# Kernel optimization log

Measured on AMD Instinct MI355X. Metric: run time of the kernel, lower is better.

The kernel has to match this reference:

```python
import jax, jax.numpy as jnp
import numpy as np

DIM = 2048
NUM_HEADS = 16
HEAD_DIM = DIM // NUM_HEADS
ROPE_BASE = 10000.0


def _rope_tables(seq_len, head_dim, dtype):
    # inv_freq over even indices, emb = cat(freqs, freqs) as in RoPEPositionalEncoding
    inv_freq = 1.0 / (ROPE_BASE ** (jnp.arange(0, head_dim, 2, dtype=jnp.float32) / head_dim))
    t = jnp.arange(seq_len, dtype=jnp.float32)
    freqs = jnp.outer(t, inv_freq)                      # [S, D/2]
    emb = jnp.concatenate([freqs, freqs], axis=-1)      # [S, D]
    # add head axis so tables broadcast over [B, S, H, D]
    return jnp.cos(emb)[:, None, :].astype(dtype), jnp.sin(emb)[:, None, :].astype(dtype)


def _apply_rope(x, cos, sin):
    # x: [B, S, H, D]; cos/sin: [S, 1, D]
    x1, x2 = x[..., ::2], x[..., 1::2]
    rotated = jnp.concatenate([-x2, x1], axis=-1)
    return x * cos + rotated * sin


def setup_inputs() -> dict:
    key = jax.random.key(0)
    ks = jax.random.split(key, 5)
    B, S = 2, 2048
    s = 1.0 / np.sqrt(DIM)
    return {
        "x": jax.random.normal(ks[0], (B, S, DIM), dtype=jnp.float32),
        "Wq": jax.random.normal(ks[1], (DIM, DIM), dtype=jnp.float32) * s,
        "Wk": jax.random.normal(ks[2], (DIM, DIM), dtype=jnp.float32) * s,
        "Wv": jax.random.normal(ks[3], (DIM, DIM), dtype=jnp.float32) * s,
        "Wo": jax.random.normal(ks[4], (DIM, DIM), dtype=jnp.float32) * s,
    }


def reference(x, Wq, Wk, Wv, Wo):
    B, S, _ = x.shape
    H, D = NUM_HEADS, HEAD_DIM
    scale = D ** -0.5

    q = (x @ Wq.T).reshape(B, S, H, D)
    k = (x @ Wk.T).reshape(B, S, H, D)
    v = (x @ Wv.T).reshape(B, S, H, D)

    cos, sin = _rope_tables(S, D, x.dtype)
    q = _apply_rope(q, cos, sin)
    k = _apply_rope(k, cos, sin)

    # [B, H, S, D]
    q = q.transpose(0, 2, 1, 3)
    k = k.transpose(0, 2, 1, 3)
    v = v.transpose(0, 2, 1, 3)

    scores = jnp.einsum("bhqd,bhkd->bhqk", q, k) * scale
    causal = jnp.tril(jnp.ones((S, S), dtype=bool))
    scores = jnp.where(causal, scores, -jnp.inf)
    attn = jax.nn.softmax(scores, axis=-1)

    out = jnp.einsum("bhqk,bhkd->bhqd", attn, v)
    out = out.transpose(0, 2, 1, 3).reshape(B, S, H * D)
    return out @ Wo.T
```

## Files before the change

kernel.cpp:

```cpp
#include <hip/hip_runtime.h>
#include <math.h>

#define DIM   2048
#define NH    16
#define HD    128
#define BB    2
#define SS    2048
#define MTOT  4096
#define NT    32

typedef unsigned short u16;
typedef short bf16x8 __attribute__((ext_vector_type(8)));
typedef float f32x4  __attribute__((ext_vector_type(4)));

typedef const void __attribute__((address_space(1)))* gas_ptr;
typedef void __attribute__((address_space(3)))* las_ptr;

__device__ __forceinline__ u16 f2bf(float f){
  union { float f; unsigned u; } v; v.f = f;
  unsigned r = v.u + 0x7FFFu + ((v.u >> 16) & 1u);
  return (u16)(r >> 16);
}
__device__ __forceinline__ float bf2f(u16 h){
  union { unsigned u; float f; } v; v.u = ((unsigned)h) << 16;
  return v.f;
}

__global__ __launch_bounds__(256) void cvt_all(
    const float* __restrict__ x,  const float* __restrict__ wq,
    const float* __restrict__ wk, const float* __restrict__ wv,
    u16* __restrict__ xb, u16* __restrict__ w0, u16* __restrict__ w1, u16* __restrict__ w2){
  int i = blockIdx.x * 256 + threadIdx.x;
  const float* src; u16* dst; int j;
  if (i < 2097152) { src = x; dst = xb; j = i; }
  else {
    int k = i - 2097152;
    int seg = k >> 20;
    j = k & 1048575;
    src = (seg == 0) ? wq : (seg == 1 ? wk : wv);
    dst = (seg == 0) ? w0 : (seg == 1 ? w1 : w2);
  }
  float4 v = ((const float4*)src)[j];
  ushort4 o;
  o.x = f2bf(v.x); o.y = f2bf(v.y); o.z = f2bf(v.z); o.w = f2bf(v.w);
  ((ushort4*)dst)[j] = o;
}

__global__ __launch_bounds__(256) void cvt_kernel(const float* __restrict__ in,
                                                  u16* __restrict__ out, int n4){
  int i = blockIdx.x * blockDim.x + threadIdx.x;
  if (i >= n4) return;
  float4 v = ((const float4*)in)[i];
  ushort4 o;
  o.x = f2bf(v.x); o.y = f2bf(v.y); o.z = f2bf(v.z); o.w = f2bf(v.w);
  ((ushort4*)out)[i] = o;
}

template<bool STORE_BF16>
__global__ __launch_bounds__(512, 2) void gemm256(
    const u16* __restrict__ A,
    const u16* __restrict__ B0, const u16* __restrict__ B1, const u16* __restrict__ B2,
    void* __restrict__ C0, void* __restrict__ C1, void* __restrict__ C2)
{
  __shared__ __align__(16) u16 Ar[2][2][256 * 32];
  __shared__ __align__(16) u16 Br[2][2][256 * 32];

  const int tid  = threadIdx.x;
  const int lane = tid & 63;
  const int wave = tid >> 6;
  const int wm   = wave >> 2;
  const int wn   = wave & 3;
  const int lg   = lane >> 4;
  const int lr   = lane & 15;

  const int cpx = gridDim.x >> 3;
  const int wg  = (blockIdx.x & 7) * cpx + (blockIdx.x >> 3);
  const int z   = wg >> 7;
  const int rem = wg & 127;
  const int m0  = (rem >> 3) * 256;
  const int n0  = (rem & 7) * 256;

  const u16* Bm = (z == 0) ? B0 : (z == 1 ? B1 : B2);
  void* Cm      = (z == 0) ? C0 : (z == 1 ? C1 : C2);
  const u16* Asrc = A  + (size_t)m0 * DIM;
  const u16* Bsrc = Bm + (size_t)n0 * DIM;

  f32x4 acc[8][4];
#pragma unroll
  for (int m = 0; m < 8; ++m)
#pragma unroll
    for (int n = 0; n < 4; ++n) acc[m][n] = (f32x4)0.0f;
  bf16x8 breg[4];

  auto stage = [&](const u16* src, u16* ldsreg, int kabs) {
#pragma unroll
    for (int it = 0; it < 2; ++it) {
      int c   = it * 512 + tid;
      int st  = c >> 4;
      int row = ((st >> 2) << 4) + (c & 15);
      int k   = kabs + ((st & 3) << 3);
      const u16* g = src + (size_t)row * DIM + k;
      char* l = (char*)ldsreg + (it * 512 + wave * 64) * 16;
      __builtin_amdgcn_global_load_lds((gas_ptr)g, (las_ptr)l, 16, 0, 0);
    }
  };

  stage(Asrc, Ar[0][0], 0);
  stage(Bsrc, Br[0][0], 0);
  stage(Asrc, Ar[0][1], 32);
  stage(Bsrc, Br[0][1], 32);
  asm volatile("s_waitcnt vmcnt(4)" ::: "memory");
  __builtin_amdgcn_s_barrier();

#define GPHASE(QQ, KK, GG)                                                              \
  {                                                                                     \
    const u16* Ab_ = Ar[b][KK];                                                         \
    const u16* Bb_ = Br[b][KK];                                                         \
    bf16x8 a0 = *(const bf16x8*)((const char*)Ab_ + ((((wm*8 + GG*4 + 0)*4 + lg) << 8) + (lr << 4))); \
    bf16x8 a1 = *(const bf16x8*)((const char*)Ab_ + ((((wm*8 + GG*4 + 1)*4 + lg) << 8) + (lr << 4))); \
    bf16x8 a2 = *(const bf16x8*)((const char*)Ab_ + ((((wm*8 + GG*4 + 2)*4 + lg) << 8) + (lr << 4))); \
    bf16x8 a3 = *(const bf16x8*)((const char*)Ab_ + ((((wm*8 + GG*4 + 3)*4 + lg) << 8) + (lr << 4))); \
    if (GG == 0) {                                                                      \
      _Pragma("unroll")                                                                 \
      for (int n_ = 0; n_ < 4; ++n_)                                                    \
        breg[n_] = *(const bf16x8*)((const char*)Bb_ + ((((wn*4 + n_)*4 + lg) << 8) + (lr << 4))); \
    }                                                                                   \
    if (t + 1 < NT) {                                                                   \
      if (QQ == 0) stage(Asrc, Ar[b ^ 1][0], (t + 1) * 64);                             \
      if (QQ == 1) stage(Bsrc, Br[b ^ 1][0], (t + 1) * 64);                             \
      if (QQ == 2) stage(Asrc, Ar[b ^ 1][1], (t + 1) * 64 + 32);                        \
      if (QQ == 3) stage(Bsrc, Br[b ^ 1][1], (t + 1) * 64 + 32);                        \
    }                                                                                   \
    __builtin_amdgcn_s_barrier();                                                       \
    asm volatile("s_waitcnt lgkmcnt(0)" ::: "memory");                                  \
    __builtin_amdgcn_sched_barrier(0);                                                  \
    __builtin_amdgcn_s_setprio(1);                                                      \
    {                                                                                   \
      acc[GG*4+0][0] = __builtin_amdgcn_mfma_f32_16x16x32_bf16(a0, breg[0], acc[GG*4+0][0], 0,0,0); \
      acc[GG*4+0][1] = __builtin_amdgcn_mfma_f32_16x16x32_bf16(a0, breg[1], acc[GG*4+0][1], 0,0,0); \
      acc[GG*4+0][2] = __builtin_amdgcn_mfma_f32_16x16x32_bf16(a0, breg[2], acc[GG*4+0][2], 0,0,0); \
      acc[GG*4+0][3] = __builtin_amdgcn_mfma_f32_16x16x32_bf16(a0, breg[3], acc[GG*4+0][3], 0,0,0); \
      acc[GG*4+1][0] = __builtin_amdgcn_mfma_f32_16x16x32_bf16(a1, breg[0], acc[GG*4+1][0], 0,0,0); \
      acc[GG*4+1][1] = __builtin_amdgcn_mfma_f32_16x16x32_bf16(a1, breg[1], acc[GG*4+1][1], 0,0,0); \
      acc[GG*4+1][2] = __builtin_amdgcn_mfma_f32_16x16x32_bf16(a1, breg[2], acc[GG*4+1][2], 0,0,0); \
      acc[GG*4+1][3] = __builtin_amdgcn_mfma_f32_16x16x32_bf16(a1, breg[3], acc[GG*4+1][3], 0,0,0); \
      acc[GG*4+2][0] = __builtin_amdgcn_mfma_f32_16x16x32_bf16(a2, breg[0], acc[GG*4+2][0], 0,0,0); \
      acc[GG*4+2][1] = __builtin_amdgcn_mfma_f32_16x16x32_bf16(a2, breg[1], acc[GG*4+2][1], 0,0,0); \
      acc[GG*4+2][2] = __builtin_amdgcn_mfma_f32_16x16x32_bf16(a2, breg[2], acc[GG*4+2][2], 0,0,0); \
      acc[GG*4+2][3] = __builtin_amdgcn_mfma_f32_16x16x32_bf16(a2, breg[3], acc[GG*4+2][3], 0,0,0); \
      acc[GG*4+3][0] = __builtin_amdgcn_mfma_f32_16x16x32_bf16(a3, breg[0], acc[GG*4+3][0], 0,0,0); \
      acc[GG*4+3][1] = __builtin_amdgcn_mfma_f32_16x16x32_bf16(a3, breg[1], acc[GG*4+3][1], 0,0,0); \
      acc[GG*4+3][2] = __builtin_amdgcn_mfma_f32_16x16x32_bf16(a3, breg[2], acc[GG*4+3][2], 0,0,0); \
      acc[GG*4+3][3] = __builtin_amdgcn_mfma_f32_16x16x32_bf16(a3, breg[3], acc[GG*4+3][3], 0,0,0); \
    }                                                                                   \
    __builtin_amdgcn_s_setprio(0);                                                      \
    if (QQ == 1) {                                                                      \
      if (t + 1 < NT) { asm volatile("s_waitcnt vmcnt(4)" ::: "memory"); }              \
      else            { asm volatile("s_waitcnt vmcnt(0)" ::: "memory"); }              \
    }                                                                                   \
    if (QQ == 3) {                                                                      \
      if (t + 1 < NT) { asm volatile("s_waitcnt vmcnt(4)" ::: "memory"); }              \
    }                                                                                   \
    __builtin_amdgcn_s_barrier();                                                       \
  }

  for (int t = 0; t < NT; ++t) {
    const int b = t & 1;
    GPHASE(0, 0, 0)
    GPHASE(1, 0, 1)
    GPHASE(2, 1, 0)
    GPHASE(3, 1, 1)
  }
#undef GPHASE

#pragma unroll
  for (int mf = 0; mf < 8; ++mf) {
    int grow = m0 + wm * 128 + mf * 16 + lg * 4;
#pragma unroll
    for (int nf = 0; nf < 4; ++nf) {
      int gcol = n0 + wn * 64 + nf * 16 + lr;
#pragma unroll
      for (int r = 0; r < 4; ++r) {
        float val = acc[mf][nf][r];
        if (STORE_BF16) ((u16*)Cm)[(size_t)(grow + r) * DIM + gcol]   = f2bf(val);
        else            ((float*)Cm)[(size_t)(grow + r) * DIM + gcol] = val;
      }
    }
  }
}

__global__ __launch_bounds__(256) void rope_kernel(u16* __restrict__ Q, u16* __restrict__ Kt){
  int gid  = blockIdx.x * 4 + (threadIdx.x >> 6);
  int lane = threadIdx.x & 63;
  int h = gid & (NH - 1);
  int s = (gid >> 4) & (SS - 1);
  int b = gid >> 15;
  size_t base = ((size_t)(b * SS + s)) * DIM + (size_t)h * HD;

  float ang = (float)s * __expf(-(float)lane * 0.14391156831212787f);
  float c, sn;
  sincosf(ang, &sn, &c);
  int jh = lane >> 1;
  int par = lane & 1;

  unsigned pq = *(const unsigned*)(Q + base + 2 * lane);
  float qe = bf2f((u16)(pq & 0xffff)), qo = bf2f((u16)(pq >> 16));
  float qa  = __shfl(qe, jh),      qb  = __shfl(qo, jh);
  float qa2 = __shfl(qe, 32 + jh), qb2 = __shfl(qo, 32 + jh);
  float qxj   = par ? qb  : qa;
  float qxj64 = par ? qb2 : qa2;
  u16 q_lo = f2bf(qxj   * c - qo * sn);
  u16 q_hi = f2bf(qxj64 * c + qe * sn);

  unsigned pk = *(const unsigned*)(Kt + base + 2 * lane);
  float ke = bf2f((u16)(pk & 0xffff)), ko = bf2f((u16)(pk >> 16));
  float ka  = __shfl(ke, jh),      kb  = __shfl(ko, jh);
  float ka2 = __shfl(ke, 32 + jh), kb2 = __shfl(ko, 32 + jh);
  float kxj   = par ? kb  : ka;
  float kxj64 = par ? kb2 : ka2;
  u16 k_lo = f2bf(kxj   * c - ko * sn);
  u16 k_hi = f2bf(kxj64 * c + ke * sn);

  Q [base + lane] = q_lo;  Q [base + 64 + lane] = q_hi;
  Kt[base + lane] = k_lo;  Kt[base + 64 + lane] = k_hi;
}

__global__ __launch_bounds__(256) void transpose_v(const u16* __restrict__ V,
                                                   u16* __restrict__ VT){
  __shared__ __align__(16) u16 T[64 * 64];
  const int tid = threadIdx.x;
  const int s0 = blockIdx.x * 64;
  const int d0 = blockIdx.y * 64;
  const int bh = blockIdx.z;
  const int b = bh >> 4, h = bh & 15;

#pragma unroll
  for (int it = 0; it < 2; ++it) {
    int c = it * 256 + tid;
    int s = c >> 3, cc = c & 7;
    uint4 v = *(const uint4*)(V + (size_t)(b * SS + s0 + s) * DIM + h * HD + d0 + cc * 8);
    *(uint4*)((char*)T + s * 128 + (((cc ^ (s & 7)) & 7) << 4)) = v;
  }
  __syncthreads();
#pragma unroll
  for (int it = 0; it < 2; ++it) {
    int c = it * 256 + tid;
    int d = c >> 3, sc = c & 7;
    u16 tmp[8];
#pragma unroll
    for (int j = 0; j < 8; ++j) {
      int s = sc * 8 + j;
      tmp[j] = *(const u16*)((char*)T + s * 128 + ((((d >> 3) ^ (s & 7)) & 7) << 4) + (d & 7) * 2);
    }
    *(uint4*)(VT + (size_t)bh * HD * SS + (size_t)(d0 + d) * SS + s0 + sc * 8) = *(const uint4*)tmp;
  }
}

#define SCALE 0.08838834764831845f

__global__ __launch_bounds__(512) void attn_kernel(
    const u16* __restrict__ Q, const u16* __restrict__ Kg, const u16* __restrict__ VT,
    u16* __restrict__ AO)
{
  __shared__ __align__(16) u16 Klds[2][64 * 128];
  __shared__ __align__(16) u16 Vlds[2][128 * 64];
  __shared__ __align__(16) u16 Plds[8][16 * 64];

  const int tid  = threadIdx.x;
  const int lane = tid & 63;
  const int w    = tid >> 6;
  const int lg   = lane >> 4;
  const int lr   = lane & 15;
  const int pair = blockIdx.x;
  const int bh   = blockIdx.y;
  const int b    = bh >> 4, h = bh & 15;
  const size_t headoff = (size_t)b * SS * DIM + (size_t)h * HD;
  const u16* VTh = VT + (size_t)bh * HD * SS;

  for (int half = 0; half < 2; ++half) {
    const int Qt = half ? (15 - pair) : pair;
    const int qbase = Qt * 128;
    const int nkv = Qt * 2 + 2;

    bf16x8 qf[4];
    {
      const u16* qrow = Q + headoff + (size_t)(qbase + w * 16 + lr) * DIM;
#pragma unroll
      for (int kf = 0; kf < 4; ++kf)
        qf[kf] = *(const bf16x8*)(qrow + kf * 32 + lg * 8);
    }

    f32x4 o_acc[8];
#pragma unroll
    for (int nf = 0; nf < 8; ++nf) o_acc[nf] = (f32x4)0.0f;
    float mrow[4] = {-INFINITY, -INFINITY, -INFINITY, -INFINITY};
    float lrow[4] = {0.f, 0.f, 0.f, 0.f};

    int cur = 0;

#define STAGE(BUF, T)                                                              \
    {                                                                              \
      const int kv0s = (T) * 64;                                                   \
      _Pragma("unroll")                                                            \
      for (int it = 0; it < 2; ++it) {                                             \
        int c = it * 512 + tid;                                                    \
        int r = c >> 4, slot = c & 15;                                             \
        int cc = slot ^ (r & 7);                                                   \
        const u16* ga = Kg + headoff + (size_t)(kv0s + r) * DIM + cc * 8;          \
        char* la = (char*)Klds[BUF] + (it * 512 + w * 64) * 16;                    \
        __builtin_amdgcn_global_load_lds((gas_ptr)ga, (las_ptr)la, 16, 0, 0);      \
      }                                                                            \
      _Pragma("unroll")                                                            \
      for (int it = 0; it < 2; ++it) {                                             \
        int c = it * 512 + tid;                                                    \
        int d = c >> 3, slot = c & 7;                                              \
        int cc = slot ^ (d & 7);                                                   \
        const u16* gv = VTh + (size_t)d * SS + kv0s + cc * 8;                      \
        char* lv = (char*)Vlds[BUF] + (it * 512 + w * 64) * 16;                    \
        __builtin_amdgcn_global_load_lds((gas_ptr)gv, (las_ptr)lv, 16, 0, 0);      \
      }                                                                            \
    }

    STAGE(0, 0);
    __syncthreads();

    for (int t = 0; t < nkv; ++t) {
      const int kv0 = t * 64;
      if (t + 1 < nkv) STAGE(cur ^ 1, t + 1);

      if (kv0 <= qbase + w * 16 + 15) {
        f32x4 sacc[4];
#pragma unroll
        for (int sf = 0; sf < 4; ++sf) {
          sacc[sf] = (f32x4)0.0f;
          int row = sf * 16 + lr;
          int sw = row & 7;
#pragma unroll
          for (int kf = 0; kf < 4; ++kf) {
            int cc = kf * 4 + lg;
            bf16x8 kfrag = *(const bf16x8*)((char*)Klds[cur] + row * 256 + ((cc ^ sw) << 4));
            sacc[sf] = __builtin_amdgcn_mfma_f32_16x16x32_bf16(qf[kf], kfrag, sacc[sf], 0, 0, 0);
          }
        }

        float p[4][4];
        float mt[4];
#pragma unroll
        for (int r = 0; r < 4; ++r) {
          int qrow = qbase + w * 16 + lg * 4 + r;
          float mx = -INFINITY;
#pragma unroll
          for (int sf = 0; sf < 4; ++sf) {
            float v = sacc[sf][r] * SCALE;
            if (kv0 + sf * 16 + lr > qrow) v = -INFINITY;
            p[sf][r] = v;
            mx = fmaxf(mx, v);
          }
          mx = fmaxf(mx, __shfl_xor(mx, 1));
          mx = fmaxf(mx, __shfl_xor(mx, 2));
          mx = fmaxf(mx, __shfl_xor(mx, 4));
          mx = fmaxf(mx, __shfl_xor(mx, 8));
          mt[r] = mx;
        }
        float alpha[4];
#pragma unroll
        for (int r = 0; r < 4; ++r) {
          float mn = fmaxf(mrow[r], mt[r]);
          alpha[r] = __expf(mrow[r] - mn);
          mrow[r] = mn;
        }
#pragma unroll
        for (int r = 0; r < 4; ++r) {
          float s = 0.f;
#pragma unroll
          for (int sf = 0; sf < 4; ++sf) {
            float pv = __expf(p[sf][r] - mrow[r]);
            p[sf][r] = pv;
            s += pv;
          }
          s += __shfl_xor(s, 1);
          s += __shfl_xor(s, 2);
          s += __shfl_xor(s, 4);
          s += __shfl_xor(s, 8);
          lrow[r] = lrow[r] * alpha[r] + s;
        }
#pragma unroll
        for (int nf = 0; nf < 8; ++nf)
#pragma unroll
          for (int r = 0; r < 4; ++r) o_acc[nf][r] *= alpha[r];

#pragma unroll
        for (int sf = 0; sf < 4; ++sf)
#pragma unroll
          for (int r = 0; r < 4; ++r) {
            int row = lg * 4 + r, col = sf * 16 + lr;
            int byteoff = (row * 128 + col * 2) ^ ((row & 7) << 4);
            *(u16*)((char*)Plds[w] + byteoff) = f2bf(p[sf][r]);
          }

#pragma unroll
        for (int ks = 0; ks < 2; ++ks) {
          bf16x8 pfrag = *(const bf16x8*)((char*)Plds[w] + ((lr * 128 + ks * 64 + lg * 16) ^ ((lr & 7) << 4)));
#pragma unroll
          for (int nf = 0; nf < 8; ++nf) {
            int vrow = nf * 16 + lr;
            int cc = ks * 4 + lg;
            bf16x8 vfrag = *(const bf16x8*)((char*)Vlds[cur] + vrow * 128 + ((cc ^ (vrow & 7)) << 4));
            o_acc[nf] = __builtin_amdgcn_mfma_f32_16x16x32_bf16(pfrag, vfrag, o_acc[nf], 0, 0, 0);
          }
        }
      }

      __syncthreads();
      cur ^= 1;
    }

    float inv[4];
#pragma unroll
    for (int r = 0; r < 4; ++r) inv[r] = 1.0f / lrow[r];
#pragma unroll
    for (int nf = 0; nf < 8; ++nf)
#pragma unroll
      for (int r = 0; r < 4; ++r) {
        int grow = qbase + w * 16 + lg * 4 + r;
        int col  = nf * 16 + lr;
        AO[(size_t)(b * SS + grow) * DIM + h * HD + col] = f2bf(o_acc[nf][r] * inv[r]);
      }
#undef STAGE
  }
}

extern "C" void kernel_launch(void* const* d_in, const int* in_sizes, int n_in,
                              void* d_out, int out_size, void* d_ws, size_t ws_size,
                              hipStream_t stream)
{
  const float* x  = (const float*)d_in[0];
  const float* Wq = (const float*)d_in[1];
  const float* Wk = (const float*)d_in[2];
  const float* Wv = (const float*)d_in[3];
  const float* Wo = (const float*)d_in[4];
  float* out = (float*)d_out;

  char* ws = (char*)d_ws;
  const size_t XB_BYTES = (size_t)MTOT * DIM * 2;
  const size_t W_BYTES  = (size_t)DIM * DIM * 2;
  u16* xb = (u16*)ws;
  u16* w0 = (u16*)(ws + XB_BYTES);
  u16* w1 = (u16*)(ws + XB_BYTES + W_BYTES);
  u16* w2 = (u16*)(ws + XB_BYTES + 2 * W_BYTES);
  u16* Qb = (u16*)(ws + XB_BYTES + 3 * W_BYTES);
  u16* Kb = Qb + (size_t)MTOT * DIM;
  u16* Vb = Kb + (size_t)MTOT * DIM;
  u16* AO = xb;
  u16* VTb = w1;

  cvt_all<<<20480, 256, 0, stream>>>(x, Wq, Wk, Wv, xb, w0, w1, w2);

  gemm256<true><<<dim3(384), 512, 0, stream>>>(xb, w0, w1, w2,
                                               (void*)Qb, (void*)Kb, (void*)Vb);

  transpose_v<<<dim3(32, 2, 32), 256, 0, stream>>>(Vb, VTb);

  rope_kernel<<<16384, 256, 0, stream>>>(Qb, Kb);

  cvt_kernel<<<4096, 256, 0, stream>>>(Wo, w0, 1048576);

  attn_kernel<<<dim3(8, 32), 512, 0, stream>>>(Qb, Kb, VTb, AO);

  gemm256<false><<<dim3(128), 512, 0, stream>>>(AO, w0, w0, w0,
                                                (void*)out, (void*)out, (void*)out);
}
```

Before: 489.4 us.

## Deepen GEMM load pipeline to four-stage ring with 32-wide K tiles

Replaces the double-buffered GEMM pipeline, which used 64-wide K steps split into two halves, with a four-buffer ring of 32-wide K tiles that are prefetched three iterations ahead. Each iteration issues half-tile loads for A and B in two phases and waits with vmcnt so more global loads stay in flight. The intent is to hide global memory latency better behind the MFMA work. The cost is a different barrier pattern and more careful vmcnt accounting at the tail, which the change handles explicitly for the last three iterations.

```diff
diff --git a/kernel.cpp b/kernel.cpp
--- a/kernel.cpp
+++ b/kernel.cpp
@@ -7,7 +7,7 @@
 #define BB    2
 #define SS    2048
 #define MTOT  4096
-#define NT    32
+#define NTK   64
 
 typedef unsigned short u16;
 typedef short bf16x8 __attribute__((ext_vector_type(8)));
@@ -62,8 +62,8 @@
     const u16* __restrict__ B0, const u16* __restrict__ B1, const u16* __restrict__ B2,
     void* __restrict__ C0, void* __restrict__ C1, void* __restrict__ C2)
 {
-  __shared__ __align__(16) u16 Ar[2][2][256 * 32];
-  __shared__ __align__(16) u16 Br[2][2][256 * 32];
+  __shared__ __align__(16) u16 Abuf[4][2][4096];
+  __shared__ __align__(16) u16 Bbuf[4][2][4096];
 
   const int tid  = threadIdx.x;
   const int lane = tid & 63;
@@ -92,86 +92,69 @@
     for (int n = 0; n < 4; ++n) acc[m][n] = (f32x4)0.0f;
   bf16x8 breg[4];
 
-  auto stage = [&](const u16* src, u16* ldsreg, int kabs) {
-#pragma unroll
-    for (int it = 0; it < 2; ++it) {
-      int c   = it * 512 + tid;
-      int st  = c >> 4;
-      int row = ((st >> 2) << 4) + (c & 15);
-      int k   = kabs + ((st & 3) << 3);
-      const u16* g = src + (size_t)row * DIM + k;
-      char* l = (char*)ldsreg + (it * 512 + wave * 64) * 16;
-      __builtin_amdgcn_global_load_lds((gas_ptr)g, (las_ptr)l, 16, 0, 0);
-    }
+  auto stageHalf = [&](const u16* src, int rowbase, int kt, u16* lds) {
+    int s   = tid >> 4;
+    int m16 = s >> 2, k8 = s & 3;
+    int row = rowbase + m16 * 16 + (tid & 15);
+    const u16* g = src + (size_t)row * DIM + kt * 32 + k8 * 8;
+    char* l = (char*)lds + wave * 1024 + lane * 16;
+    __builtin_amdgcn_global_load_lds((gas_ptr)g, (las_ptr)l, 16, 0, 0);
   };
 
-  stage(Asrc, Ar[0][0], 0);
-  stage(Bsrc, Br[0][0], 0);
-  stage(Asrc, Ar[0][1], 32);
-  stage(Bsrc, Br[0][1], 32);
-  asm volatile("s_waitcnt vmcnt(4)" ::: "memory");
+#pragma unroll
+  for (int pt = 0; pt < 3; ++pt) {
+    stageHalf(Asrc, 0,   pt, Abuf[pt][0]);
+    stageHalf(Bsrc, 0,   pt, Bbuf[pt][0]);
+    stageHalf(Asrc, 128, pt, Abuf[pt][1]);
+    stageHalf(Bsrc, 128, pt, Bbuf[pt][1]);
+  }
+  asm volatile("s_waitcnt vmcnt(8)" ::: "memory");
   __builtin_amdgcn_s_barrier();
 
-#define GPHASE(QQ, KK, GG)                                                              \
+#define PH(Q)                                                                           \
   {                                                                                     \
-    const u16* Ab_ = Ar[b][KK];                                                         \
-    const u16* Bb_ = Br[b][KK];                                                         \
-    bf16x8 a0 = *(const bf16x8*)((const char*)Ab_ + ((((wm*8 + GG*4 + 0)*4 + lg) << 8) + (lr << 4))); \
-    bf16x8 a1 = *(const bf16x8*)((const char*)Ab_ + ((((wm*8 + GG*4 + 1)*4 + lg) << 8) + (lr << 4))); \
-    bf16x8 a2 = *(const bf16x8*)((const char*)Ab_ + ((((wm*8 + GG*4 + 2)*4 + lg) << 8) + (lr << 4))); \
-    bf16x8 a3 = *(const bf16x8*)((const char*)Ab_ + ((((wm*8 + GG*4 + 3)*4 + lg) << 8) + (lr << 4))); \
-    if (GG == 0) {                                                                      \
+    bf16x8 a_[4];                                                                       \
+    _Pragma("unroll")                                                                   \
+    for (int m = 0; m < 4; ++m)                                                         \
+      a_[m] = *(const bf16x8*)((const char*)Ah + ((((Q*4 + m)*4 + lg) << 8) + (lr << 4))); \
+    if (Q == 0) {                                                                       \
       _Pragma("unroll")                                                                 \
-      for (int n_ = 0; n_ < 4; ++n_)                                                    \
-        breg[n_] = *(const bf16x8*)((const char*)Bb_ + ((((wn*4 + n_)*4 + lg) << 8) + (lr << 4))); \
+      for (int nf = 0; nf < 4; ++nf)                                                    \
+        breg[nf] = *(const bf16x8*)((const char*)Bh + (((((wn & 1)*4 + nf)*4 + lg) << 8) + (lr << 4))); \
     }                                                                                   \
-    if (t + 1 < NT) {                                                                   \
-      if (QQ == 0) stage(Asrc, Ar[b ^ 1][0], (t + 1) * 64);                             \
-      if (QQ == 1) stage(Bsrc, Br[b ^ 1][0], (t + 1) * 64);                             \
-      if (QQ == 2) stage(Asrc, Ar[b ^ 1][1], (t + 1) * 64 + 32);                        \
-      if (QQ == 3) stage(Bsrc, Br[b ^ 1][1], (t + 1) * 64 + 32);                        \
+    if (doStage) {                                                                      \
+      stageHalf(Asrc, Q * 128, t + 3, Abuf[sb][Q]);                                     \
+      stageHalf(Bsrc, Q * 128, t + 3, Bbuf[sb][Q]);                                     \
     }                                                                                   \
     __builtin_amdgcn_s_barrier();                                                       \
     asm volatile("s_waitcnt lgkmcnt(0)" ::: "memory");                                  \
     __builtin_amdgcn_sched_barrier(0);                                                  \
     __builtin_amdgcn_s_setprio(1);                                                      \
-    {                                                                                   \
-      acc[GG*4+0][0] = __builtin_amdgcn_mfma_f32_16x16x32_bf16(a0, breg[0], acc[GG*4+0][0], 0,0,0); \
-      acc[GG*4+0][1] = __builtin_amdgcn_mfma_f32_16x16x32_bf16(a0, breg[1], acc[GG*4+0][1], 0,0,0); \
-      acc[GG*4+0][2] = __builtin_amdgcn_mfma_f32_16x16x32_bf16(a0, breg[2], acc[GG*4+0][2], 0,0,0); \
-      acc[GG*4+0][3] = __builtin_amdgcn_mfma_f32_16x16x32_bf16(a0, breg[3], acc[GG*4+0][3], 0,0,0); \
-      acc[GG*4+1][0] = __builtin_amdgcn_mfma_f32_16x16x32_bf16(a1, breg[0], acc[GG*4+1][0], 0,0,0); \
-      acc[GG*4+1][1] = __builtin_amdgcn_mfma_f32_16x16x32_bf16(a1, breg[1], acc[GG*4+1][1], 0,0,0); \
-      acc[GG*4+1][2] = __builtin_amdgcn_mfma_f32_16x16x32_bf16(a1, breg[2], acc[GG*4+1][2], 0,0,0); \
-      acc[GG*4+1][3] = __builtin_amdgcn_mfma_f32_16x16x32_bf16(a1, breg[3], acc[GG*4+1][3], 0,0,0); \
-      acc[GG*4+2][0] = __builtin_amdgcn_mfma_f32_16x16x32_bf16(a2, breg[0], acc[GG*4+2][0], 0,0,0); \
-      acc[GG*4+2][1] = __builtin_amdgcn_mfma_f32_16x16x32_bf16(a2, breg[1], acc[GG*4+2][1], 0,0,0); \
-      acc[GG*4+2][2] = __builtin_amdgcn_mfma_f32_16x16x32_bf16(a2, breg[2], acc[GG*4+2][2], 0,0,0); \
-      acc[GG*4+2][3] = __builtin_amdgcn_mfma_f32_16x16x32_bf16(a2, breg[3], acc[GG*4+2][3], 0,0,0); \
-      acc[GG*4+3][0] = __builtin_amdgcn_mfma_f32_16x16x32_bf16(a3, breg[0], acc[GG*4+3][0], 0,0,0); \
-      acc[GG*4+3][1] = __builtin_amdgcn_mfma_f32_16x16x32_bf16(a3, breg[1], acc[GG*4+3][1], 0,0,0); \
-      acc[GG*4+3][2] = __builtin_amdgcn_mfma_f32_16x16x32_bf16(a3, breg[2], acc[GG*4+3][2], 0,0,0); \
-      acc[GG*4+3][3] = __builtin_amdgcn_mfma_f32_16x16x32_bf16(a3, breg[3], acc[GG*4+3][3], 0,0,0); \
-    }                                                                                   \
+    _Pragma("unroll")                                                                   \
+    for (int m = 0; m < 4; ++m)                                                         \
+      _Pragma("unroll")                                                                 \
+      for (int nf = 0; nf < 4; ++nf)                                                    \
+        acc[Q*4 + m][nf] = __builtin_amdgcn_mfma_f32_16x16x32_bf16(a_[m], breg[nf], acc[Q*4 + m][nf], 0, 0, 0); \
     __builtin_amdgcn_s_setprio(0);                                                      \
-    if (QQ == 1) {                                                                      \
-      if (t + 1 < NT) { asm volatile("s_waitcnt vmcnt(4)" ::: "memory"); }              \
-      else            { asm volatile("s_waitcnt vmcnt(0)" ::: "memory"); }              \
-    }                                                                                   \
-    if (QQ == 3) {                                                                      \
-      if (t + 1 < NT) { asm volatile("s_waitcnt vmcnt(4)" ::: "memory"); }              \
-    }                                                                                   \
-    __builtin_amdgcn_s_barrier();                                                       \
-  }
-
-  for (int t = 0; t < NT; ++t) {
-    const int b = t & 1;
-    GPHASE(0, 0, 0)
-    GPHASE(1, 0, 1)
-    GPHASE(2, 1, 0)
-    GPHASE(3, 1, 1)
-  }
-#undef GPHASE
+  }
+
+  for (int t = 0; t < NTK; ++t) {
+    const int buf = t & 3;
+    const int sb  = (t + 3) & 3;
+    const bool doStage = (t + 3) < NTK;
+    const u16* Ah = Abuf[buf][wm];
+    const u16* Bh = Bbuf[buf][wn >> 1];
+
+    PH(0)
+    __builtin_amdgcn_s_barrier();
+
+    PH(1)
+    if (t < NTK - 3)       { asm volatile("s_waitcnt vmcnt(8)" ::: "memory"); }
+    else if (t == NTK - 3) { asm volatile("s_waitcnt vmcnt(4)" ::: "memory"); }
+    else if (t == NTK - 2) { asm volatile("s_waitcnt vmcnt(0)" ::: "memory"); }
+    __builtin_amdgcn_s_barrier();
+  }
+#undef PH
 
 #pragma unroll
   for (int mf = 0; mf < 8; ++mf) {
```

After: 470.6 us. 3.8% less time.
